# Optimization experiments

Hardware: AMD Instinct MI355X
Metric: run time of the kernel (lower is better)

Reference implementation:

```python
import jax, jax.numpy as jnp
import numpy as np

N = 100000      # nodes
E = 1200000     # edges
D_IN = 7        # node feature dim
H = 64          # hidden_dim
G = 64          # graphs in batch
L = 2           # num_layers
EPS = 1e-5      # BatchNorm eps


def setup_inputs() -> dict:
    key = jax.random.key(0)
    ks = jax.random.split(key, 16)
    s = 1.0 / np.sqrt(H)
    return {
        "x": jax.random.normal(ks[0], (N, D_IN), jnp.float32),
        "edge_index": jax.random.randint(ks[1], (2, E), 0, N, dtype=jnp.int32),
        "batch": jnp.sort(jax.random.randint(ks[2], (N,), 0, G, dtype=jnp.int32)),
        "W_in": jax.random.normal(ks[3], (D_IN, H), jnp.float32) / np.sqrt(D_IN),
        "b_in": jax.random.normal(ks[4], (H,), jnp.float32) * 0.01,
        "conv_W": jax.random.normal(ks[5], (L, H, H), jnp.float32) * s,
        "conv_b": jax.random.normal(ks[6], (L, H), jnp.float32) * 0.01,
        "bn_gamma": jax.random.uniform(ks[7], (L, H), jnp.float32, 0.5, 1.5),
        "bn_beta": jax.random.normal(ks[8], (L, H), jnp.float32) * 0.1,
        "bn_mean": jax.random.normal(ks[9], (L, H), jnp.float32) * 0.1,
        "bn_var": jax.random.uniform(ks[10], (L, H), jnp.float32, 0.5, 1.5),
        "mlp_W1": jax.random.normal(ks[11], (H, H // 2), jnp.float32) * s,
        "mlp_b1": jax.random.normal(ks[12], (H // 2,), jnp.float32) * 0.01,
        "mlp_W2": jax.random.normal(ks[13], (H // 2, 1), jnp.float32) / np.sqrt(H // 2),
        "mlp_b2": jax.random.normal(ks[14], (1,), jnp.float32) * 0.01,
    }


def _gcn_conv(h, edge_index, W, b):
    # PyG GCNConv (eval): add self-loops, symmetric deg^{-1/2} normalization.
    n = h.shape[0]
    loops = jnp.arange(n, dtype=edge_index.dtype)
    src = jnp.concatenate([edge_index[0], loops])
    dst = jnp.concatenate([edge_index[1], loops])
    deg = jax.ops.segment_sum(jnp.ones_like(src, h.dtype), dst, num_segments=n)
    dinv = jnp.where(deg > 0, jax.lax.rsqrt(jnp.maximum(deg, 1.0)), 0.0)
    hw = h @ W                                  # [N, H]
    norm = (dinv[src] * dinv[dst])[:, None]     # [E+N, 1]
    msg = hw[src] * norm                        # gather + scale
    out = jax.ops.segment_sum(msg, dst, num_segments=n)  # scatter-add
    return out + b


def reference(x, edge_index, batch, W_in, b_in, conv_W, conv_b,
              bn_gamma, bn_beta, bn_mean, bn_var,
              mlp_W1, mlp_b1, mlp_W2, mlp_b2):
    # input projection (dropout is identity in eval mode)
    h = jax.nn.relu(x @ W_in + b_in)
    for i in range(L):
        hn = _gcn_conv(h, edge_index, conv_W[i], conv_b[i])
        # BatchNorm1d in inference mode with running stats
        hn = (hn - bn_mean[i]) * jax.lax.rsqrt(bn_var[i] + EPS) * bn_gamma[i] + bn_beta[i]
        hn = jax.nn.relu(hn)
        h = h + hn if i > 0 else hn
    # global_mean_pool over batch segment ids
    sums = jax.ops.segment_sum(h, batch, num_segments=G)        # [G, H]
    cnt = jax.ops.segment_sum(jnp.ones((h.shape[0],), h.dtype), batch, num_segments=G)
    pooled = sums / jnp.maximum(cnt, 1.0)[:, None]
    z = jax.nn.relu(pooled @ mlp_W1 + mlp_b1)
    return z @ mlp_W2 + mlp_b2                                  # [G, 1]
```

## Files before the change

### kernel.cpp

```cpp
#include <hip/hip_runtime.h>

#define NN 100000
#define NE 1200000
#define DIN 7
#define H 64
#define NG 64

#define NT 196
#define TILE 512
#define CAPT2 6912
#define PB 128
#define PCH (NE / PB)

typedef float v2f __attribute__((ext_vector_type(2)));

static __device__ __forceinline__ unsigned int pk_fp8(float a, float b, float c, float d) {
    int r = __builtin_amdgcn_cvt_pk_fp8_f32(a, b, 0, false);
    r = __builtin_amdgcn_cvt_pk_fp8_f32(c, d, r, true);
    return (unsigned int)r;
}

#define ZWORDS (NT + NG * H + NG)
__global__ __launch_bounds__(256) void k_zero(int* __restrict__ z) {
    int i = blockIdx.x * 256 + threadIdx.x;
    if (i < ZWORDS) z[i] = 0;
}

__global__ __launch_bounds__(256) void k_psort(const int* __restrict__ src, const int* __restrict__ dst,
                                               unsigned int* __restrict__ buck, int* __restrict__ tcur) {
    __shared__ unsigned int lbuf[PCH];
    __shared__ unsigned char tileof[PCH];
    __shared__ int hist[NT];
    __shared__ int lstart[NT];
    __shared__ int ldelta[NT];
    __shared__ int sc[256];
    int tid = threadIdx.x;
    int e0 = blockIdx.x * PCH;
    for (int i = tid; i < NT; i += 256) hist[i] = 0;
    __syncthreads();
    for (int i = tid; i < PCH; i += 256)
        atomicAdd(&hist[dst[e0 + i] >> 9], 1);
    __syncthreads();
    int hv = (tid < NT) ? hist[tid] : 0;
    sc[tid] = hv; __syncthreads();
    for (int off = 1; off < 256; off <<= 1) {
        int y = (tid >= off) ? sc[tid - off] : 0;
        __syncthreads(); sc[tid] += y; __syncthreads();
    }
    if (tid < NT) lstart[tid] = sc[tid] - hv;
    __syncthreads();
    if (tid < NT) hist[tid] = lstart[tid];
    __syncthreads();
    for (int i = tid; i < PCH; i += 256) {
        int d = dst[e0 + i], s = src[e0 + i];
        int t = d >> 9;
        int pos = atomicAdd(&hist[t], 1);
        lbuf[pos] = ((unsigned)(d & 511) << 17) | (unsigned)s;
        tileof[pos] = (unsigned char)t;
    }
    __syncthreads();
    if (tid < NT) {
        int n = hist[tid] - lstart[tid];
        int g = (n > 0) ? atomicAdd(&tcur[tid], n) : 0;
        ldelta[tid] = g - lstart[tid];
    }
    __syncthreads();
    for (int i = tid; i < PCH; i += 256) {
        int t = tileof[i];
        int off = ldelta[t] + i;
        if (off < CAPT2) buck[(size_t)t * CAPT2 + off] = lbuf[i];
    }
}

__global__ __launch_bounds__(256) void k_tile_csr(const unsigned int* __restrict__ buck,
                                                  const int* __restrict__ tcur,
                                                  int* __restrict__ row_ptr, float* __restrict__ dinv,
                                                  int* __restrict__ col) {
    __shared__ int hist[TILE];
    __shared__ int lcur[TILE];
    __shared__ int sc[256];
    __shared__ int colbuf[CAPT2];
    int t = blockIdx.x, tid = threadIdx.x;
    int tv = (tid < NT) ? tcur[tid] : 0;
    sc[tid] = tv; __syncthreads();
    for (int off = 1; off < 256; off <<= 1) {
        int y = (tid >= off) ? sc[tid - off] : 0;
        __syncthreads(); sc[tid] += y; __syncthreads();
    }
    int gb = (t == 0) ? 0 : sc[t - 1];
    int n = tcur[t];
    if (n > CAPT2) n = CAPT2;
    const unsigned int* b = buck + (size_t)t * CAPT2;
    __syncthreads();
    for (int i = tid; i < TILE; i += 256) hist[i] = 0;
    __syncthreads();
    for (int i = tid; i < n; i += 256) atomicAdd(&hist[b[i] >> 17], 1);
    __syncthreads();
    int a0 = hist[2 * tid], a1 = hist[2 * tid + 1];
    int s = a0 + a1;
    sc[tid] = s; __syncthreads();
    for (int off = 1; off < 256; off <<= 1) {
        int y = (tid >= off) ? sc[tid - off] : 0;
        __syncthreads(); sc[tid] += y; __syncthreads();
    }
    int excl = sc[tid] - s;
    int g0 = t * TILE + 2 * tid, g1 = g0 + 1;
    if (g0 <= NN) row_ptr[g0] = gb + excl;
    if (g1 <= NN) row_ptr[g1] = gb + excl + a0;
    if (g0 < NN) dinv[g0] = rsqrtf((float)(a0 + 1));
    if (g1 < NN) dinv[g1] = rsqrtf((float)(a1 + 1));
    lcur[2 * tid] = excl; lcur[2 * tid + 1] = excl + a0;
    __syncthreads();
    for (int i = tid; i < n; i += 256) {
        unsigned int w = b[i];
        int p = atomicAdd(&lcur[w >> 17], 1);
        colbuf[p] = (int)(w & 0x1FFFFu);
    }
    __syncthreads();
    for (int i = tid; i < n; i += 256) col[gb + i] = colbuf[i];
}

__global__ __launch_bounds__(256) void k_gemm0_fused(const float* __restrict__ x,
                                                     const float* __restrict__ Win, const float* __restrict__ bin,
                                                     const float* __restrict__ W0, const float* __restrict__ dinv,
                                                     unsigned int* __restrict__ hws8) {
    __shared__ float xs[64][8];
    __shared__ float wsin[DIN * 64];
    __shared__ float bs[64];
    __shared__ __align__(16) float As[64][68];
    __shared__ __align__(16) float Wc[64][64];
    int tid = threadIdx.x;
    int r0 = blockIdx.x * 64;

    for (int idx = tid; idx < 64 * DIN; idx += 256) {
        int r = idx / DIN, k = idx - r * DIN;
        int gr = r0 + r;
        xs[r][k] = (gr < NN) ? x[gr * DIN + k] : 0.f;
    }
    for (int idx = tid; idx < DIN * 64; idx += 256) wsin[idx] = Win[idx];
    if (tid < 64) bs[tid] = bin[tid];
    for (int idx = tid; idx < 64 * 64; idx += 256) Wc[idx >> 6][idx & 63] = W0[idx];
    __syncthreads();

    {
        int r = tid >> 2, q = tid & 3;
        float xr[DIN];
#pragma unroll
        for (int k = 0; k < DIN; k++) xr[k] = xs[r][k];
#pragma unroll
        for (int cc = 0; cc < 16; cc++) {
            int c = q * 16 + cc;
            float a = bs[c];
#pragma unroll
            for (int k = 0; k < DIN; k++) a += xr[k] * wsin[k * 64 + c];
            As[c][r] = fmaxf(a, 0.f);
        }
    }
    __syncthreads();

    int tr = tid >> 4, tc = tid & 15;
    float acc[4][4] = {};
#pragma unroll 4
    for (int kk = 0; kk < 64; kk++) {
        float a0 = As[kk][tr * 4 + 0], a1 = As[kk][tr * 4 + 1];
        float a2 = As[kk][tr * 4 + 2], a3 = As[kk][tr * 4 + 3];
        float4 bv = *(const float4*)&Wc[kk][tc * 4];
        acc[0][0] += a0 * bv.x; acc[0][1] += a0 * bv.y; acc[0][2] += a0 * bv.z; acc[0][3] += a0 * bv.w;
        acc[1][0] += a1 * bv.x; acc[1][1] += a1 * bv.y; acc[1][2] += a1 * bv.z; acc[1][3] += a1 * bv.w;
        acc[2][0] += a2 * bv.x; acc[2][1] += a2 * bv.y; acc[2][2] += a2 * bv.z; acc[2][3] += a2 * bv.w;
        acc[3][0] += a3 * bv.x; acc[3][1] += a3 * bv.y; acc[3][2] += a3 * bv.z; acc[3][3] += a3 * bv.w;
    }
#pragma unroll
    for (int i = 0; i < 4; i++) {
        int gr = r0 + tr * 4 + i;
        if (gr < NN) {
            float s = dinv[gr];
            hws8[gr * 16 + tc] = pk_fp8(acc[i][0] * s, acc[i][1] * s, acc[i][2] * s, acc[i][3] * s);
        }
    }
}

__global__ __launch_bounds__(256) void k_gemm_scale(const float* __restrict__ A, const float* __restrict__ W,
                                                    const float* __restrict__ dinv,
                                                    unsigned int* __restrict__ hws8) {
    __shared__ __align__(16) float As[64][68];
    __shared__ __align__(16) float Ws[64][64];
    int tid = threadIdx.x;
    int r0 = blockIdx.x * 64;
    int row = tid >> 2, q = tid & 3;
    int gr0 = r0 + row;
#pragma unroll
    for (int j = 0; j < 4; j++) {
        int c = q * 16 + j * 4;
        float4 av = make_float4(0.f, 0.f, 0.f, 0.f);
        if (gr0 < NN) av = *(const float4*)(A + gr0 * H + c);
        As[c + 0][row] = av.x; As[c + 1][row] = av.y;
        As[c + 2][row] = av.z; As[c + 3][row] = av.w;
        *(float4*)&Ws[row][c] = *(const float4*)(W + row * H + c);
    }
    __syncthreads();

    int tr = tid >> 4, tc = tid & 15;
    float acc[4][4] = {};
#pragma unroll 4
    for (int kk = 0; kk < 64; kk++) {
        float a0 = As[kk][tr * 4 + 0], a1 = As[kk][tr * 4 + 1];
        float a2 = As[kk][tr * 4 + 2], a3 = As[kk][tr * 4 + 3];
        float4 bv = *(const float4*)&Ws[kk][tc * 4];
        acc[0][0] += a0 * bv.x; acc[0][1] += a0 * bv.y; acc[0][2] += a0 * bv.z; acc[0][3] += a0 * bv.w;
        acc[1][0] += a1 * bv.x; acc[1][1] += a1 * bv.y; acc[1][2] += a1 * bv.z; acc[1][3] += a1 * bv.w;
        acc[2][0] += a2 * bv.x; acc[2][1] += a2 * bv.y; acc[2][2] += a2 * bv.z; acc[2][3] += a2 * bv.w;
        acc[3][0] += a3 * bv.x; acc[3][1] += a3 * bv.y; acc[3][2] += a3 * bv.z; acc[3][3] += a3 * bv.w;
    }
#pragma unroll
    for (int i = 0; i < 4; i++) {
        int gr = r0 + tr * 4 + i;
        if (gr < NN) {
            float s = dinv[gr];
            hws8[gr * 16 + tc] = pk_fp8(acc[i][0] * s, acc[i][1] * s, acc[i][2] * s, acc[i][3] * s);
        }
    }
}

__global__ __launch_bounds__(256) void k_agg(const unsigned int* __restrict__ hws8,
                                             const int* __restrict__ row_ptr,
                                             const int* __restrict__ col, const float* __restrict__ dinv,
                                             const float* __restrict__ cb, const float* __restrict__ gamma,
                                             const float* __restrict__ beta, const float* __restrict__ mean,
                                             const float* __restrict__ var, float* __restrict__ h, int layer) {
    int tid = threadIdx.x;
    int sub = tid & 7;
    int v = blockIdx.x * 32 + (tid >> 3);
    const uint2* rb = (const uint2*)hws8;

    uint2 w = rb[v * 8 + sub];
    v2f p0 = __builtin_amdgcn_cvt_pk_f32_fp8((int)w.x, false);
    v2f p1 = __builtin_amdgcn_cvt_pk_f32_fp8((int)w.x, true);
    v2f p2 = __builtin_amdgcn_cvt_pk_f32_fp8((int)w.y, false);
    v2f p3 = __builtin_amdgcn_cvt_pk_f32_fp8((int)w.y, true);
    float a0 = p0.x, a1 = p0.y, a2 = p1.x, a3 = p1.y;
    float a4 = p2.x, a5 = p2.y, a6 = p3.x, a7 = p3.y;

    int s = row_ptr[v], e = row_ptr[v + 1];
    int i = s;
    for (; i + 4 <= e; i += 4) {
        int u0 = col[i], u1 = col[i + 1], u2 = col[i + 2], u3 = col[i + 3];
        uint2 w0 = rb[u0 * 8 + sub];
        uint2 w1 = rb[u1 * 8 + sub];
        uint2 w2 = rb[u2 * 8 + sub];
        uint2 w3 = rb[u3 * 8 + sub];
#pragma unroll
        for (int k = 0; k < 4; k++) {
            uint2 wk = (k == 0) ? w0 : (k == 1) ? w1 : (k == 2) ? w2 : w3;
            v2f q0 = __builtin_amdgcn_cvt_pk_f32_fp8((int)wk.x, false);
            v2f q1 = __builtin_amdgcn_cvt_pk_f32_fp8((int)wk.x, true);
            v2f q2 = __builtin_amdgcn_cvt_pk_f32_fp8((int)wk.y, false);
            v2f q3 = __builtin_amdgcn_cvt_pk_f32_fp8((int)wk.y, true);
            a0 += q0.x; a1 += q0.y; a2 += q1.x; a3 += q1.y;
            a4 += q2.x; a5 += q2.y; a6 += q3.x; a7 += q3.y;
        }
    }
    for (; i < e; ++i) {
        uint2 wu = rb[col[i] * 8 + sub];
        v2f q0 = __builtin_amdgcn_cvt_pk_f32_fp8((int)wu.x, false);
        v2f q1 = __builtin_amdgcn_cvt_pk_f32_fp8((int)wu.x, true);
        v2f q2 = __builtin_amdgcn_cvt_pk_f32_fp8((int)wu.y, false);
        v2f q3 = __builtin_amdgcn_cvt_pk_f32_fp8((int)wu.y, true);
        a0 += q0.x; a1 += q0.y; a2 += q1.x; a3 += q1.y;
        a4 += q2.x; a5 += q2.y; a6 += q3.x; a7 += q3.y;
    }

    float dv = dinv[v];
    int f0 = sub * 8;
    float4 cb0 = *(const float4*)(cb + f0),    cb1 = *(const float4*)(cb + f0 + 4);
    float4 mn0 = *(const float4*)(mean + f0),  mn1 = *(const float4*)(mean + f0 + 4);
    float4 vr0 = *(const float4*)(var + f0),   vr1 = *(const float4*)(var + f0 + 4);
    float4 gm0 = *(const float4*)(gamma + f0), gm1 = *(const float4*)(gamma + f0 + 4);
    float4 bt0 = *(const float4*)(beta + f0),  bt1 = *(const float4*)(beta + f0 + 4);

    float r0 = (a0 * dv + cb0.x - mn0.x) * rsqrtf(vr0.x + 1e-5f) * gm0.x + bt0.x;
    float r1 = (a1 * dv + cb0.y - mn0.y) * rsqrtf(vr0.y + 1e-5f) * gm0.y + bt0.y;
    float r2 = (a2 * dv + cb0.z - mn0.z) * rsqrtf(vr0.z + 1e-5f) * gm0.z + bt0.z;
    float r3 = (a3 * dv + cb0.w - mn0.w) * rsqrtf(vr0.w + 1e-5f) * gm0.w + bt0.w;
    float r4 = (a4 * dv + cb1.x - mn1.x) * rsqrtf(vr1.x + 1e-5f) * gm1.x + bt1.x;
    float r5 = (a5 * dv + cb1.y - mn1.y) * rsqrtf(vr1.y + 1e-5f) * gm1.y + bt1.y;
    float r6 = (a6 * dv + cb1.z - mn1.z) * rsqrtf(vr1.z + 1e-5f) * gm1.z + bt1.z;
    float r7 = (a7 * dv + cb1.w - mn1.w) * rsqrtf(vr1.w + 1e-5f) * gm1.w + bt1.w;
    r0 = fmaxf(r0, 0.f); r1 = fmaxf(r1, 0.f); r2 = fmaxf(r2, 0.f); r3 = fmaxf(r3, 0.f);
    r4 = fmaxf(r4, 0.f); r5 = fmaxf(r5, 0.f); r6 = fmaxf(r6, 0.f); r7 = fmaxf(r7, 0.f);
    if (layer) {
        float4 hp0 = *(const float4*)(h + v * H + f0);
        float4 hp1 = *(const float4*)(h + v * H + f0 + 4);
        r0 += hp0.x; r1 += hp0.y; r2 += hp0.z; r3 += hp0.w;
        r4 += hp1.x; r5 += hp1.y; r6 += hp1.z; r7 += hp1.w;
    }
    *(float4*)(h + v * H + f0) = make_float4(r0, r1, r2, r3);
    *(float4*)(h + v * H + f0 + 4) = make_float4(r4, r5, r6, r7);
}

#define POOL_CHUNK 32
__global__ __launch_bounds__(64) void k_pool(const float* __restrict__ h, const int* __restrict__ batch,
                                             float* __restrict__ sums, float* __restrict__ cntg) {
    int lane = threadIdx.x;
    int start = blockIdx.x * POOL_CHUNK;
    int end = start + POOL_CHUNK; if (end > NN) end = NN;
    float acc = 0.f, c = 0.f;
    int curg = batch[start];
    for (int n = start; n < end; ++n) {
        int g = batch[n];
        if (g != curg) {
            atomicAdd(&sums[curg * H + lane], acc);
            if (lane == 0) atomicAdd(&cntg[curg], c);
            acc = 0.f; c = 0.f; curg = g;
        }
        acc += h[n * H + lane];
        c += 1.f;
    }
    atomicAdd(&sums[curg * H + lane], acc);
    if (lane == 0) atomicAdd(&cntg[curg], c);
}

__global__ __launch_bounds__(64) void k_mlp(const float* __restrict__ sums, const float* __restrict__ cntg,
                                            const float* __restrict__ W1, const float* __restrict__ b1,
                                            const float* __restrict__ W2, const float* __restrict__ b2,
                                            float* __restrict__ out) {
    int g = threadIdx.x;
    float inv = 1.f / fmaxf(cntg[g], 1.f);
    float pooled[H];
#pragma unroll
    for (int k = 0; k < H; k++) pooled[k] = sums[g * H + k] * inv;
    float o = b2[0];
#pragma unroll
    for (int j = 0; j < H / 2; j++) {
        float z = b1[j];
#pragma unroll
        for (int k = 0; k < H; k++) z += pooled[k] * W1[k * (H / 2) + j];
        o += fmaxf(z, 0.f) * W2[j];
    }
    out[g] = o;
}

extern "C" void kernel_launch(void* const* d_in, const int* in_sizes, int n_in,
                              void* d_out, int out_size, void* d_ws, size_t ws_size,
                              hipStream_t stream) {
    const float* x     = (const float*)d_in[0];
    const int*   ei    = (const int*)d_in[1];
    const int*   batch = (const int*)d_in[2];
    const float* Win   = (const float*)d_in[3];
    const float* bin   = (const float*)d_in[4];
    const float* convW = (const float*)d_in[5];
    const float* convb = (const float*)d_in[6];
    const float* gamma = (const float*)d_in[7];
    const float* beta  = (const float*)d_in[8];
    const float* mean  = (const float*)d_in[9];
    const float* var   = (const float*)d_in[10];
    const float* W1    = (const float*)d_in[11];
    const float* b1    = (const float*)d_in[12];
    const float* W2    = (const float*)d_in[13];
    const float* b2    = (const float*)d_in[14];
    float* out = (float*)d_out;

    char* p = (char*)d_ws;
    auto alloc = [&](size_t bytes) -> void* {
        void* r = (void*)p;
        p += (bytes + 255) & ~(size_t)255;
        return r;
    };
    float*          h       = (float*)alloc((size_t)NN * H * 4);
    unsigned int*   hws8    = (unsigned int*)alloc((size_t)NN * 16 * 4);
    float*          dinv    = (float*)alloc((size_t)NN * 4);
    int*            row_ptr = (int*)alloc((size_t)(NN + 1) * 4);
    int*            col     = (int*)alloc((size_t)NE * 4);
    unsigned int*   buck    = (unsigned int*)alloc((size_t)NT * CAPT2 * 4);
    int*            zbase   = (int*)alloc((size_t)ZWORDS * 4);
    int*            tcur    = zbase;
    float*          sums    = (float*)(zbase + NT);
    float*          cntg    = (float*)(zbase + NT + NG * H);

    const int* src  = ei;
    const int* dstp = ei + NE;

    k_zero<<<(ZWORDS + 255) / 256, 256, 0, stream>>>(zbase);

    k_psort<<<PB, 256, 0, stream>>>(src, dstp, buck, tcur);
    k_tile_csr<<<NT, 256, 0, stream>>>(buck, tcur, row_ptr, dinv, col);

    k_gemm0_fused<<<(NN + 63) / 64, 256, 0, stream>>>(x, Win, bin, convW, dinv, hws8);
    k_agg<<<NN / 32, 256, 0, stream>>>(hws8, row_ptr, col, dinv,
                                       convb, gamma, beta, mean, var, h, 0);
    k_gemm_scale<<<(NN + 63) / 64, 256, 0, stream>>>(h, convW + H * H, dinv, hws8);
    k_agg<<<NN / 32, 256, 0, stream>>>(hws8, row_ptr, col, dinv,
                                       convb + H, gamma + H, beta + H,
                                       mean + H, var + H, h, 1);

    k_pool<<<(NN + POOL_CHUNK - 1) / POOL_CHUNK, 64, 0, stream>>>(h, batch, sums, cntg);
    k_mlp<<<1, 64, 0, stream>>>(sums, cntg, W1, b1, W2, b2, out);
}
```

Before: 184.0 us.

## Degree-sort nodes within each tile to balance aggregation work per wavefront

The CSR build kernel now counting-sorts each tile's nodes by in-degree (capped at 63) and writes a node permutation. The aggregation kernels read their node index through this permutation, so the 8-lane groups in a wavefront handle nodes of similar degree and loop-trip divergence shrinks. In exchange the CSR kernel does extra shared-memory scans and atomics, and the aggregation adds an indirect load and less contiguous output writes.

```diff
diff --git a/kernel.cpp b/kernel.cpp
--- a/kernel.cpp
+++ b/kernel.cpp
@@ -75,11 +75,14 @@
 __global__ __launch_bounds__(256) void k_tile_csr(const unsigned int* __restrict__ buck,
                                                   const int* __restrict__ tcur,
                                                   int* __restrict__ row_ptr, float* __restrict__ dinv,
-                                                  int* __restrict__ col) {
+                                                  int* __restrict__ col, int* __restrict__ norder) {
     __shared__ int hist[TILE];
     __shared__ int lcur[TILE];
     __shared__ int sc[256];
     __shared__ int colbuf[CAPT2];
+    __shared__ int dhist[64];
+    __shared__ int dbase[64];
+    __shared__ unsigned short ordbuf[TILE];
     int t = blockIdx.x, tid = threadIdx.x;
     int tv = (tid < NT) ? tcur[tid] : 0;
     sc[tid] = tv; __syncthreads();
@@ -93,6 +96,7 @@
     const unsigned int* b = buck + (size_t)t * CAPT2;
     __syncthreads();
     for (int i = tid; i < TILE; i += 256) hist[i] = 0;
+    if (tid < 64) dhist[tid] = 0;
     __syncthreads();
     for (int i = tid; i < n; i += 256) atomicAdd(&hist[b[i] >> 17], 1);
     __syncthreads();
@@ -110,7 +114,22 @@
     if (g0 < NN) dinv[g0] = rsqrtf((float)(a0 + 1));
     if (g1 < NN) dinv[g1] = rsqrtf((float)(a1 + 1));
     lcur[2 * tid] = excl; lcur[2 * tid + 1] = excl + a0;
-    __syncthreads();
+    int b0 = (a0 < 63) ? a0 : 63, b1 = (a1 < 63) ? a1 : 63;
+    if (g0 < NN) atomicAdd(&dhist[b0], 1);
+    if (g1 < NN) atomicAdd(&dhist[b1], 1);
+    __syncthreads();
+    if (tid < 64) dbase[tid] = dhist[tid];
+    __syncthreads();
+    for (int off = 1; off < 64; off <<= 1) {
+        int y = (tid >= off && tid < 64) ? dbase[tid - off] : 0;
+        __syncthreads();
+        if (tid < 64) dbase[tid] += y;
+        __syncthreads();
+    }
+    if (tid < 64) dbase[tid] -= dhist[tid];
+    __syncthreads();
+    if (g0 < NN) { int r = atomicAdd(&dbase[b0], 1); ordbuf[r] = (unsigned short)(2 * tid); }
+    if (g1 < NN) { int r = atomicAdd(&dbase[b1], 1); ordbuf[r] = (unsigned short)(2 * tid + 1); }
     for (int i = tid; i < n; i += 256) {
         unsigned int w = b[i];
         int p = atomicAdd(&lcur[w >> 17], 1);
@@ -118,6 +137,8 @@
     }
     __syncthreads();
     for (int i = tid; i < n; i += 256) col[gb + i] = colbuf[i];
+    int lim = NN - t * TILE; if (lim > TILE) lim = TILE;
+    for (int i = tid; i < lim; i += 256) norder[t * TILE + i] = t * TILE + (int)ordbuf[i];
 }
 
 __global__ __launch_bounds__(256) void k_gemm0_fused(const float* __restrict__ x,
@@ -225,12 +246,13 @@
 __global__ __launch_bounds__(256) void k_agg(const unsigned int* __restrict__ hws8,
                                              const int* __restrict__ row_ptr,
                                              const int* __restrict__ col, const float* __restrict__ dinv,
+                                             const int* __restrict__ norder,
                                              const float* __restrict__ cb, const float* __restrict__ gamma,
                                              const float* __restrict__ beta, const float* __restrict__ mean,
                                              const float* __restrict__ var, float* __restrict__ h, int layer) {
     int tid = threadIdx.x;
     int sub = tid & 7;
-    int v = blockIdx.x * 32 + (tid >> 3);
+    int v = norder[blockIdx.x * 32 + (tid >> 3)];
     const uint2* rb = (const uint2*)hws8;
 
     uint2 w = rb[v * 8 + sub];
@@ -371,6 +393,7 @@
     float*          dinv    = (float*)alloc((size_t)NN * 4);
     int*            row_ptr = (int*)alloc((size_t)(NN + 1) * 4);
     int*            col     = (int*)alloc((size_t)NE * 4);
+    int*            norder  = (int*)alloc((size_t)NN * 4);
     unsigned int*   buck    = (unsigned int*)alloc((size_t)NT * CAPT2 * 4);
     int*            zbase   = (int*)alloc((size_t)ZWORDS * 4);
     int*            tcur    = zbase;
@@ -383,13 +406,13 @@
     k_zero<<<(ZWORDS + 255) / 256, 256, 0, stream>>>(zbase);
 
     k_psort<<<PB, 256, 0, stream>>>(src, dstp, buck, tcur);
-    k_tile_csr<<<NT, 256, 0, stream>>>(buck, tcur, row_ptr, dinv, col);
+    k_tile_csr<<<NT, 256, 0, stream>>>(buck, tcur, row_ptr, dinv, col, norder);
 
     k_gemm0_fused<<<(NN + 63) / 64, 256, 0, stream>>>(x, Win, bin, convW, dinv, hws8);
-    k_agg<<<NN / 32, 256, 0, stream>>>(hws8, row_ptr, col, dinv,
+    k_agg<<<NN / 32, 256, 0, stream>>>(hws8, row_ptr, col, dinv, norder,
                                        convb, gamma, beta, mean, var, h, 0);
     k_gemm_scale<<<(NN + 63) / 64, 256, 0, stream>>>(h, convW + H * H, dinv, hws8);
-    k_agg<<<NN / 32, 256, 0, stream>>>(hws8, row_ptr, col, dinv,
+    k_agg<<<NN / 32, 256, 0, stream>>>(hws8, row_ptr, col, dinv, norder,
                                        convb + H, gamma + H, beta + H,
                                        mean + H, var + H, h, 1);
 
```

Result: slower. 196.0 us (+6.5%).

## Fuse mean-pool and MLP into one per-graph kernel using binary search

Applied to the files above, without the earlier changes.

Replaces the atomic chunked pooling kernel and the separate single-block MLP kernel with one kernel that launches a block per graph. Each block binary-searches the sorted batch array to find its node range, reduces the rows across four waves, and then runs the MLP in shared memory. This removes the global atomics, one kernel launch and the zeroing of the sums and count buffers. In exchange, pooling now runs on only 64 blocks, so it relies on far less parallelism to stream the hidden features.

```diff
diff --git a/kernel.cpp b/kernel.cpp
--- a/kernel.cpp
+++ b/kernel.cpp
@@ -20,10 +20,9 @@
     return (unsigned int)r;
 }
 
-#define ZWORDS (NT + NG * H + NG)
 __global__ __launch_bounds__(256) void k_zero(int* __restrict__ z) {
-    int i = blockIdx.x * 256 + threadIdx.x;
-    if (i < ZWORDS) z[i] = 0;
+    int i = threadIdx.x;
+    if (i < NT) z[i] = 0;
 }
 
 __global__ __launch_bounds__(256) void k_psort(const int* __restrict__ src, const int* __restrict__ dst,
@@ -298,46 +297,46 @@
     *(float4*)(h + v * H + f0 + 4) = make_float4(r4, r5, r6, r7);
 }
 
-#define POOL_CHUNK 32
-__global__ __launch_bounds__(64) void k_pool(const float* __restrict__ h, const int* __restrict__ batch,
-                                             float* __restrict__ sums, float* __restrict__ cntg) {
-    int lane = threadIdx.x;
-    int start = blockIdx.x * POOL_CHUNK;
-    int end = start + POOL_CHUNK; if (end > NN) end = NN;
-    float acc = 0.f, c = 0.f;
-    int curg = batch[start];
-    for (int n = start; n < end; ++n) {
-        int g = batch[n];
-        if (g != curg) {
-            atomicAdd(&sums[curg * H + lane], acc);
-            if (lane == 0) atomicAdd(&cntg[curg], c);
-            acc = 0.f; c = 0.f; curg = g;
-        }
-        acc += h[n * H + lane];
-        c += 1.f;
-    }
-    atomicAdd(&sums[curg * H + lane], acc);
-    if (lane == 0) atomicAdd(&cntg[curg], c);
-}
-
-__global__ __launch_bounds__(64) void k_mlp(const float* __restrict__ sums, const float* __restrict__ cntg,
-                                            const float* __restrict__ W1, const float* __restrict__ b1,
-                                            const float* __restrict__ W2, const float* __restrict__ b2,
-                                            float* __restrict__ out) {
-    int g = threadIdx.x;
-    float inv = 1.f / fmaxf(cntg[g], 1.f);
-    float pooled[H];
-#pragma unroll
-    for (int k = 0; k < H; k++) pooled[k] = sums[g * H + k] * inv;
-    float o = b2[0];
-#pragma unroll
-    for (int j = 0; j < H / 2; j++) {
-        float z = b1[j];
-#pragma unroll
-        for (int k = 0; k < H; k++) z += pooled[k] * W1[k * (H / 2) + j];
-        o += fmaxf(z, 0.f) * W2[j];
-    }
-    out[g] = o;
+__global__ __launch_bounds__(256) void k_poolmlp(const float* __restrict__ h, const int* __restrict__ batch,
+                                                 const float* __restrict__ W1, const float* __restrict__ b1,
+                                                 const float* __restrict__ W2, const float* __restrict__ b2,
+                                                 float* __restrict__ out) {
+    __shared__ float psum[4][64];
+    __shared__ float pooled[64];
+    __shared__ float zz[32];
+    int g = blockIdx.x;
+    int tid = threadIdx.x;
+    int wv = tid >> 6, lane = tid & 63;
+
+    int lo = 0, r = NN;
+    while (lo < r) { int m = (lo + r) >> 1; if (batch[m] < g) lo = m + 1; else r = m; }
+    int hi = lo; r = NN;
+    while (hi < r) { int m = (hi + r) >> 1; if (batch[m] < g + 1) hi = m + 1; else r = m; }
+
+    float acc = 0.f;
+    for (int n = lo + wv; n < hi; n += 4) acc += h[n * H + lane];
+    psum[wv][lane] = acc;
+    __syncthreads();
+
+    if (tid < 64) {
+        int cnt = hi - lo;
+        float inv = (cnt > 0) ? 1.f / (float)cnt : 0.f;
+        pooled[tid] = (psum[0][tid] + psum[1][tid] + psum[2][tid] + psum[3][tid]) * inv;
+    }
+    __syncthreads();
+    if (tid < 32) {
+        float z = b1[tid];
+#pragma unroll
+        for (int k = 0; k < H; k++) z += pooled[k] * W1[k * (H / 2) + tid];
+        zz[tid] = fmaxf(z, 0.f) * W2[tid];
+    }
+    __syncthreads();
+    if (tid == 0) {
+        float o = b2[0];
+#pragma unroll
+        for (int j = 0; j < 32; j++) o += zz[j];
+        out[g] = o;
+    }
 }
 
 extern "C" void kernel_launch(void* const* d_in, const int* in_sizes, int n_in,
@@ -372,15 +371,12 @@
     int*            row_ptr = (int*)alloc((size_t)(NN + 1) * 4);
     int*            col     = (int*)alloc((size_t)NE * 4);
     unsigned int*   buck    = (unsigned int*)alloc((size_t)NT * CAPT2 * 4);
-    int*            zbase   = (int*)alloc((size_t)ZWORDS * 4);
-    int*            tcur    = zbase;
-    float*          sums    = (float*)(zbase + NT);
-    float*          cntg    = (float*)(zbase + NT + NG * H);
+    int*            tcur    = (int*)alloc((size_t)NT * 4);
 
     const int* src  = ei;
     const int* dstp = ei + NE;
 
-    k_zero<<<(ZWORDS + 255) / 256, 256, 0, stream>>>(zbase);
+    k_zero<<<1, 256, 0, stream>>>(tcur);
 
     k_psort<<<PB, 256, 0, stream>>>(src, dstp, buck, tcur);
     k_tile_csr<<<NT, 256, 0, stream>>>(buck, tcur, row_ptr, dinv, col);
@@ -393,6 +389,5 @@
                                        convb + H, gamma + H, beta + H,
                                        mean + H, var + H, h, 1);
 
-    k_pool<<<(NN + POOL_CHUNK - 1) / POOL_CHUNK, 64, 0, stream>>>(h, batch, sums, cntg);
-    k_mlp<<<1, 64, 0, stream>>>(sums, cntg, W1, b1, W2, b2, out);
-}
+    k_poolmlp<<<NG, 256, 0, stream>>>(h, batch, W1, b1, W2, b2, out);
+}
```

After: 253.1 us. +37.6%, slower.
